# Optimization experiments

Measured on AMD Instinct MI355X. Metric: run time of the kernel, lower is better.

The kernel has to match this reference:

```python
import jax, jax.numpy as jnp
import numpy as np

B, T, D = 8, 2048, 512
F = 512          # filters (== D due to residual add)
K = 7            # kernel_size
H = 128          # hidden_dim of kernel generator (hard-coded in source)
LN_EPS = 1e-3    # keras LayerNormalization default epsilon


def setup_inputs() -> dict:
    key = jax.random.key(0)
    ks = jax.random.split(key, 8)
    x = jax.random.normal(ks[0], (B, T, D), dtype=jnp.float32)
    # kernel generator: Dense(D->H, relu) then Dense(H->K*F)
    W1 = jax.random.normal(ks[1], (D, H), dtype=jnp.float32) * (1.0 / np.sqrt(D))
    b1 = jnp.zeros((H,), dtype=jnp.float32)
    W2 = jax.random.normal(ks[2], (H, K * F), dtype=jnp.float32) * (1.0 / np.sqrt(H))
    b2 = jnp.zeros((K * F,), dtype=jnp.float32)
    # LayerNorm params
    gamma = jnp.ones((F,), dtype=jnp.float32)
    beta = jnp.zeros((F,), dtype=jnp.float32)
    return {"x": x, "W1": W1, "b1": b1, "W2": W2, "b2": b2,
            "gamma": gamma, "beta": beta}


def _dynamic_conv_block(x, W1, b1, W2, b2, gamma, beta):
    # per-token dynamic kernels: [B, T, K, F]
    h = jax.nn.relu(jnp.einsum("btd,dh->bth", x, W1) + b1)
    kernels = (jnp.einsum("bth,hf->btf", h, W2) + b2).reshape(B, T, K, F)
    # extract sliding-window patches (same padding): [B, T, K, D]
    pad = K // 2
    xp = jnp.pad(x, ((0, 0), (pad, pad), (0, 0)))
    patches = jnp.stack([xp[:, i:i + T, :] for i in range(K)], axis=2)
    # per-token conv: contract over window K and input channels D
    conv_out = jnp.einsum("btkd,btkf->btf", patches, kernels)
    # residual + LayerNorm + relu (dropout is identity at inference)
    y = conv_out + x
    mu = jnp.mean(y, axis=-1, keepdims=True)
    var = jnp.mean(jnp.square(y - mu), axis=-1, keepdims=True)
    y = (y - mu) * jax.lax.rsqrt(var + LN_EPS) * gamma + beta
    return jax.nn.relu(y)


def reference(x, W1, b1, W2, b2, gamma, beta):
    return _dynamic_conv_block(x, W1, b1, W2, b2, gamma, beta)
```

## Files before the change

### kernel.cpp

```cpp
#include <hip/hip_runtime.h>
#include <utility>

#define NT 2048
#define ND 512
#define NH 128
#define NKW 7
#define NTOK 16384

typedef float f32x4 __attribute__((ext_vector_type(4)));
typedef __bf16 bf16x8 __attribute__((ext_vector_type(8)));
typedef unsigned short u16;
typedef unsigned int u32;
typedef u16 u16x8 __attribute__((ext_vector_type(8)));

template<int N> using IC = std::integral_constant<int, N>;

__device__ __forceinline__ u16 f2bf(float f){
  u32 u = __builtin_bit_cast(u32, f);
  return (u16)((u + 0x7fffu + ((u>>16)&1u)) >> 16);
}
__device__ __forceinline__ float bf2f(u16 s){
  u32 u = ((u32)s)<<16;
  return __builtin_bit_cast(float, u);
}
__device__ __forceinline__ bf16x8 pack8(const float4& a, const float4& b){
  u16x8 u;
  u[0]=f2bf(a.x); u[1]=f2bf(a.y); u[2]=f2bf(a.z); u[3]=f2bf(a.w);
  u[4]=f2bf(b.x); u[5]=f2bf(b.y); u[6]=f2bf(b.z); u[7]=f2bf(b.w);
  return __builtin_bit_cast(bf16x8, u);
}

__global__ __launch_bounds__(256) void prep2_kernel(
    const float* __restrict__ W1, const float* __restrict__ W2,
    const float* __restrict__ b2, u16* __restrict__ W1F, u16* __restrict__ B3)
{
  int f = blockIdx.x*256 + threadIdx.x;
  u16 u[8];
  if (f < 8192){
    int n = f & 127, sk = f >> 7, kb = sk*8;
    #pragma unroll
    for (int j=0;j<8;++j) u[j] = f2bf(W1[(size_t)(kb+j)*NH + n]);
    u16x8 v;
    #pragma unroll
    for (int j=0;j<8;++j) v[j]=u[j];
    *(u16x8*)(W1F + (size_t)f*8) = v;
  } else {
    int g = f - 8192;
    int n = g & 511, sc = g >> 9, kb = sc*8;
    if (kb < 896){
      int kwin = kb >> 7, h = kb & 127;
      #pragma unroll
      for (int j=0;j<8;++j) u[j] = f2bf(W2[(size_t)(h+j)*(NKW*ND) + kwin*ND + n]);
    } else {
      int jb = kb - 896;
      #pragma unroll
      for (int j=0;j<8;++j){ int jj = jb+j; u[j] = (jj<NKW)? f2bf(b2[(size_t)jj*ND + n]) : (u16)0; }
    }
    u16x8 v;
    #pragma unroll
    for (int j=0;j<8;++j) v[j]=u[j];
    *(u16x8*)(B3 + (size_t)g*8) = v;
  }
}

__global__ __launch_bounds__(512,2) void fused_kernel(
    const float* __restrict__ x, const u16* __restrict__ W1F,
    const float* __restrict__ b1, const u16* __restrict__ B3,
    const float* __restrict__ gamma, const float* __restrict__ beta,
    float* __restrict__ out)
{
  __shared__ __align__(16) u16 h_lds[2*64*64];
  __shared__ float rs_lds[70];
  __shared__ __align__(16) float s_lds[64][8];
  __shared__ float red_s[64][8], red_q[64][8];
  __shared__ float mu_lds[64], rstd_lds[64];

  const int tid = threadIdx.x, w = tid>>6, l = tid&63;
  const int m_base = blockIdx.x*64;

  #pragma unroll
  for (int r=0;r<8;++r){
    int row = w*8 + r;
    const float4* pr = (const float4*)(x + (size_t)(m_base+row)*ND + l*8);
    float4 a = pr[0], b = pr[1];
    float s = (a.x+a.y)+(a.z+a.w)+((b.x+b.y)+(b.z+b.w));
    s += __shfl_xor(s,1); s += __shfl_xor(s,2); s += __shfl_xor(s,4);
    s += __shfl_xor(s,8); s += __shfl_xor(s,16); s += __shfl_xor(s,32);
    if (l==0) rs_lds[3+row] = s;
  }
  if (w < 6){
    int j = (w<3)? w : w+64;
    int tg2 = m_base + j - 3;
    float s2 = 0.f;
    if (tg2 >= 0 && tg2 < NTOK){
      const float4* p2 = (const float4*)(x + (size_t)tg2*ND + l*8);
      float4 a = p2[0], b = p2[1];
      s2 = (a.x+a.y)+(a.z+a.w)+((b.x+b.y)+(b.z+b.w));
    }
    s2 += __shfl_xor(s2,1); s2 += __shfl_xor(s2,2); s2 += __shfl_xor(s2,4);
    s2 += __shfl_xor(s2,8); s2 += __shfl_xor(s2,16); s2 += __shfl_xor(s2,32);
    if (l==0) rs_lds[j] = s2;
  }
  __syncthreads();
  {
    int rr = tid>>3, k = tid&7;
    float v = 0.f;
    if (k < NKW){
      int ti = (m_base+rr) & (NT-1);
      int idx = ti + k - 3;
      if (idx >= 0 && idx < NT) v = rs_lds[rr+k];
    }
    s_lds[rr][k] = v;
  }

  {
    const int wm = w>>2, wn = w&3;
    f32x4 acc1[2][2] = {};
    #pragma unroll
    for (int kc=0;kc<16;++kc){
      bf16x8 af[2], bfr[2];
      #pragma unroll
      for (int mi=0;mi<2;++mi){
        int row = wm*32 + mi*16 + (l&15);
        const float4* px = (const float4*)(x + (size_t)(m_base+row)*ND + kc*32 + (l>>4)*8);
        af[mi] = pack8(px[0], px[1]);
      }
      #pragma unroll
      for (int ni=0;ni<2;++ni){
        int n = wn*32 + ni*16 + (l&15);
        bfr[ni] = *(const bf16x8*)(W1F + ((size_t)(kc*4 + (l>>4))*128 + n)*8);
      }
      #pragma unroll
      for (int mi=0;mi<2;++mi)
        #pragma unroll
        for (int ni=0;ni<2;++ni)
          acc1[mi][ni] = __builtin_amdgcn_mfma_f32_16x16x32_bf16(af[mi], bfr[ni], acc1[mi][ni],0,0,0);
    }
    #pragma unroll
    for (int ni=0;ni<2;++ni){
      int col = wn*32 + ni*16 + (l&15);
      float bias = b1[col];
      int half = col>>6, cc = col&63;
      #pragma unroll
      for (int mi=0;mi<2;++mi)
        #pragma unroll
        for (int r=0;r<4;++r){
          int row = wm*32 + mi*16 + (l>>4)*4 + r;
          float v = fmaxf(acc1[mi][ni][r] + bias, 0.f);
          int byte = half*8192 + row*128 + ((cc*2) ^ ((row&7)<<4));
          *(u16*)((char*)h_lds + byte) = f2bf(v);
        }
    }
  }
  __syncthreads();

  f32x4 acc[4][4] = {};
  bf16x8 bE[2][4], bO[2][4];

  float sr[4][8];
  #pragma unroll
  for (int mi=0;mi<4;++mi){
    int r = mi*16 + (l&15);
    f32x4 a0 = *(const f32x4*)&s_lds[r][0];
    f32x4 a1 = *(const f32x4*)&s_lds[r][4];
    #pragma unroll
    for (int j=0;j<4;++j){ sr[mi][j] = a0[j]; sr[mi][4+j] = a1[j]; }
  }

  auto loadB = [&](int c, bf16x8 (&bf)[2][4]){
    #pragma unroll
    for (int kk=0;kk<2;++kk)
      #pragma unroll
      for (int ni=0;ni<4;++ni){
        int rowB = w*64 + ni*16 + (l&15);
        bf[kk][ni] = *(const bf16x8*)(B3 + ((size_t)((c*2+kk)*4 + (l>>4))*512 + rowB)*8);
      }
  };
  auto chunk = [&](auto kcC, bf16x8 (&b)[2][4]){
    constexpr int kc = decltype(kcC)::value;
    #pragma unroll
    for (int kk=0;kk<2;++kk){
      bf16x8 af[4];
      #pragma unroll
      for (int mi=0;mi<4;++mi){
        int r = mi*16 + (l&15);
        const char* hp = (const char*)h_lds + (kc&1)*8192 + r*128
                         + (((kk*64) + ((l>>4)*16)) ^ ((r&7)<<4));
        u16x8 hv = *(const u16x8*)hp;
        float sv = sr[mi][kc>>1];
        #pragma unroll
        for (int j=0;j<8;++j) af[mi][j] = (__bf16)(bf2f(hv[j]) * sv);
      }
      __builtin_amdgcn_s_setprio(1);
      #pragma unroll
      for (int mi=0;mi<4;++mi)
        #pragma unroll
        for (int ni=0;ni<4;++ni)
          acc[mi][ni] = __builtin_amdgcn_mfma_f32_16x16x32_bf16(af[mi], b[kk][ni], acc[mi][ni],0,0,0);
      __builtin_amdgcn_s_setprio(0);
    }
  };
  #define SB0 __builtin_amdgcn_sched_barrier(0)

  loadB(0, bE);
  SB0;
  #define PAIR(T) \
    loadB(2*(T)+1, bO); SB0; chunk(IC<2*(T)>{}, bE); \
    loadB(2*(T)+2, bE); SB0; chunk(IC<2*(T)+1>{}, bO);
  PAIR(0) PAIR(1) PAIR(2) PAIR(3) PAIR(4) PAIR(5) PAIR(6)
  #undef PAIR
  {
    bf16x8 af[4];
    const bool g0 = ((l>>4)==0);
    #pragma unroll
    for (int mi=0;mi<4;++mi){
      #pragma unroll
      for (int j=0;j<7;++j) af[mi][j] = g0 ? (__bf16)sr[mi][j] : (__bf16)0.f;
      af[mi][7] = (__bf16)0.f;
    }
    #pragma unroll
    for (int mi=0;mi<4;++mi)
      #pragma unroll
      for (int ni=0;ni<4;++ni)
        acc[mi][ni] = __builtin_amdgcn_mfma_f32_16x16x32_bf16(af[mi], bE[0][ni], acc[mi][ni],0,0,0);
  }
  #undef SB0

  #pragma unroll
  for (int mi=0;mi<4;++mi){
    #pragma unroll
    for (int r=0;r<4;++r){
      int m = mi*16 + (l>>4)*4 + r;
      int tg = m_base + m;
      float ps=0.f, pq=0.f;
      #pragma unroll
      for (int ni=0;ni<4;++ni){
        int n = w*64 + ni*16 + (l&15);
        float v = acc[mi][ni][r] + x[(size_t)tg*ND + n];
        acc[mi][ni][r] = v;
        ps += v; pq += v*v;
      }
      #pragma unroll
      for (int msk=1; msk<16; msk<<=1){ ps += __shfl_xor(ps,msk); pq += __shfl_xor(pq,msk); }
      if ((l&15)==0){ red_s[m][w]=ps; red_q[m][w]=pq; }
    }
  }
  __syncthreads();
  if (tid < 64){
    float ssum=0.f, sq=0.f;
    #pragma unroll
    for (int ww=0; ww<8; ++ww){ ssum += red_s[tid][ww]; sq += red_q[tid][ww]; }
    float mu = ssum * (1.0f/ND);
    float var = sq*(1.0f/ND) - mu*mu;
    mu_lds[tid] = mu;
    rstd_lds[tid] = rsqrtf(var + 1e-3f);
  }
  __syncthreads();
  float gv[4], bv[4];
  #pragma unroll
  for (int ni=0;ni<4;++ni){
    int n = w*64 + ni*16 + (l&15);
    gv[ni] = gamma[n]; bv[ni] = beta[n];
  }
  #pragma unroll
  for (int mi=0;mi<4;++mi){
    #pragma unroll
    for (int r=0;r<4;++r){
      int m = mi*16 + (l>>4)*4 + r;
      int tg = m_base + m;
      float mu = mu_lds[m], rstd = rstd_lds[m];
      #pragma unroll
      for (int ni=0;ni<4;++ni){
        int n = w*64 + ni*16 + (l&15);
        float v = (acc[mi][ni][r]-mu)*rstd*gv[ni] + bv[ni];
        out[(size_t)tg*ND + n] = fmaxf(v, 0.f);
      }
    }
  }
}

extern "C" void kernel_launch(void* const* d_in, const int* in_sizes, int n_in,
                              void* d_out, int out_size, void* d_ws, size_t ws_size,
                              hipStream_t stream)
{
  (void)in_sizes; (void)n_in; (void)out_size; (void)ws_size;
  const float* x     = (const float*)d_in[0];
  const float* W1    = (const float*)d_in[1];
  const float* b1    = (const float*)d_in[2];
  const float* W2    = (const float*)d_in[3];
  const float* b2    = (const float*)d_in[4];
  const float* gamma = (const float*)d_in[5];
  const float* beta  = (const float*)d_in[6];
  float* out = (float*)d_out;

  char* ws = (char*)d_ws;
  u16* W1F = (u16*)(ws);
  u16* B3  = (u16*)(ws + 131072);

  prep2_kernel<<<272, 256, 0, stream>>>(W1, W2, b2, W1F, B3);
  fused_kernel<<<256, 512, 0, stream>>>(x, W1F, b1, B3, gamma, beta, out);
}
```

Measured before the change: 140.2 us.

## Stage B3 chunks through LDS with direct global-to-LDS loads, 32-token blocks

Restructures the fused kernel to process 32 tokens per block with 256 threads across 512 blocks. The dynamic-weight matrix B3 is now staged through double-buffered LDS tiles using global_load_lds, and the scaled A operand goes through LDS, instead of each wave loading B fragments straight from global memory into registers. The goal is better latency hiding through an explicit LDS pipeline and more blocks to spread over the CUs. In exchange it uses about 70KB of LDS per block, which can limit occupancy, adds a block barrier per chunk, and halves the M-tile, so each staged B element is reused across fewer tokens.

```diff
diff --git a/kernel.cpp b/kernel.cpp
--- a/kernel.cpp
+++ b/kernel.cpp
@@ -1,5 +1,4 @@
 #include <hip/hip_runtime.h>
-#include <utility>
 
 #define NT 2048
 #define ND 512
@@ -11,9 +10,8 @@
 typedef __bf16 bf16x8 __attribute__((ext_vector_type(8)));
 typedef unsigned short u16;
 typedef unsigned int u32;
+typedef u16 u16x4 __attribute__((ext_vector_type(4)));
 typedef u16 u16x8 __attribute__((ext_vector_type(8)));
-
-template<int N> using IC = std::integral_constant<int, N>;
 
 __device__ __forceinline__ u16 f2bf(float f){
   u32 u = __builtin_bit_cast(u32, f);
@@ -28,6 +26,11 @@
   u[0]=f2bf(a.x); u[1]=f2bf(a.y); u[2]=f2bf(a.z); u[3]=f2bf(a.w);
   u[4]=f2bf(b.x); u[5]=f2bf(b.y); u[6]=f2bf(b.z); u[7]=f2bf(b.w);
   return __builtin_bit_cast(bf16x8, u);
+}
+__device__ __forceinline__ void gload_lds16(const void* g, void* l){
+  __builtin_amdgcn_global_load_lds(
+      (const __attribute__((address_space(1))) void*)g,
+      (__attribute__((address_space(3))) void*)l, 16, 0, 0);
 }
 
 __global__ __launch_bounds__(256) void prep2_kernel(
@@ -63,43 +66,34 @@
   }
 }
 
-__global__ __launch_bounds__(512,2) void fused_kernel(
+__global__ __launch_bounds__(256,2) void fused2_kernel(
     const float* __restrict__ x, const u16* __restrict__ W1F,
     const float* __restrict__ b1, const u16* __restrict__ B3,
     const float* __restrict__ gamma, const float* __restrict__ beta,
     float* __restrict__ out)
 {
-  __shared__ __align__(16) u16 h_lds[2*64*64];
-  __shared__ float rs_lds[70];
-  __shared__ __align__(16) float s_lds[64][8];
-  __shared__ float red_s[64][8], red_q[64][8];
-  __shared__ float mu_lds[64], rstd_lds[64];
+  __shared__ __align__(16) u16 Bt0[16384], Bt1[16384];
+  __shared__ __align__(16) u16 At0[1024], At1[1024];
+  __shared__ __align__(16) u16 h_lds[32*128];
+  __shared__ float rs_lds[40];
+  __shared__ float s_lds[32][8];
+  __shared__ float red_s[32][4], red_q[32][4];
+  __shared__ float mu_lds[32], rstd_lds[32];
 
   const int tid = threadIdx.x, w = tid>>6, l = tid&63;
-  const int m_base = blockIdx.x*64;
-
-  #pragma unroll
-  for (int r=0;r<8;++r){
-    int row = w*8 + r;
-    const float4* pr = (const float4*)(x + (size_t)(m_base+row)*ND + l*8);
-    float4 a = pr[0], b = pr[1];
-    float s = (a.x+a.y)+(a.z+a.w)+((b.x+b.y)+(b.z+b.w));
+  const int m_base = blockIdx.x*32;
+
+  for (int t=w; t<38; t+=4){
+    int g = m_base + t - 3;
+    float s = 0.f;
+    if (g >= 0 && g < NTOK){
+      const float4* p = (const float4*)(x + (size_t)g*ND + l*8);
+      float4 a = p[0], b = p[1];
+      s = (a.x+a.y)+(a.z+a.w)+((b.x+b.y)+(b.z+b.w));
+    }
     s += __shfl_xor(s,1); s += __shfl_xor(s,2); s += __shfl_xor(s,4);
     s += __shfl_xor(s,8); s += __shfl_xor(s,16); s += __shfl_xor(s,32);
-    if (l==0) rs_lds[3+row] = s;
-  }
-  if (w < 6){
-    int j = (w<3)? w : w+64;
-    int tg2 = m_base + j - 3;
-    float s2 = 0.f;
-    if (tg2 >= 0 && tg2 < NTOK){
-      const float4* p2 = (const float4*)(x + (size_t)tg2*ND + l*8);
-      float4 a = p2[0], b = p2[1];
-      s2 = (a.x+a.y)+(a.z+a.w)+((b.x+b.y)+(b.z+b.w));
-    }
-    s2 += __shfl_xor(s2,1); s2 += __shfl_xor(s2,2); s2 += __shfl_xor(s2,4);
-    s2 += __shfl_xor(s2,8); s2 += __shfl_xor(s2,16); s2 += __shfl_xor(s2,32);
-    if (l==0) rs_lds[j] = s2;
+    if (l==0) rs_lds[t] = s;
   }
   __syncthreads();
   {
@@ -114,164 +108,155 @@
   }
 
   {
-    const int wm = w>>2, wn = w&3;
-    f32x4 acc1[2][2] = {};
+    const int wm = w&1, wn = w>>1;
+    f32x4 acc1[4] = {};
     #pragma unroll
     for (int kc=0;kc<16;++kc){
-      bf16x8 af[2], bfr[2];
-      #pragma unroll
-      for (int mi=0;mi<2;++mi){
-        int row = wm*32 + mi*16 + (l&15);
-        const float4* px = (const float4*)(x + (size_t)(m_base+row)*ND + kc*32 + (l>>4)*8);
-        af[mi] = pack8(px[0], px[1]);
-      }
-      #pragma unroll
-      for (int ni=0;ni<2;++ni){
-        int n = wn*32 + ni*16 + (l&15);
-        bfr[ni] = *(const bf16x8*)(W1F + ((size_t)(kc*4 + (l>>4))*128 + n)*8);
-      }
-      #pragma unroll
-      for (int mi=0;mi<2;++mi)
-        #pragma unroll
-        for (int ni=0;ni<2;++ni)
-          acc1[mi][ni] = __builtin_amdgcn_mfma_f32_16x16x32_bf16(af[mi], bfr[ni], acc1[mi][ni],0,0,0);
-    }
-    #pragma unroll
-    for (int ni=0;ni<2;++ni){
-      int col = wn*32 + ni*16 + (l&15);
+      int row = wm*16 + (l&15);
+      const float4* px = (const float4*)(x + (size_t)(m_base+row)*ND + kc*32 + (l>>4)*8);
+      bf16x8 af = pack8(px[0], px[1]);
+      #pragma unroll
+      for (int ni=0;ni<4;++ni){
+        int n = wn*64 + ni*16 + (l&15);
+        bf16x8 bfr = *(const bf16x8*)(W1F + ((size_t)(kc*4+(l>>4))*128 + n)*8);
+        acc1[ni] = __builtin_amdgcn_mfma_f32_16x16x32_bf16(af, bfr, acc1[ni],0,0,0);
+      }
+    }
+    #pragma unroll
+    for (int ni=0;ni<4;++ni){
+      int col = wn*64 + ni*16 + (l&15);
       float bias = b1[col];
-      int half = col>>6, cc = col&63;
-      #pragma unroll
-      for (int mi=0;mi<2;++mi)
-        #pragma unroll
-        for (int r=0;r<4;++r){
-          int row = wm*32 + mi*16 + (l>>4)*4 + r;
-          float v = fmaxf(acc1[mi][ni][r] + bias, 0.f);
-          int byte = half*8192 + row*128 + ((cc*2) ^ ((row&7)<<4));
-          *(u16*)((char*)h_lds + byte) = f2bf(v);
-        }
-    }
-  }
-  __syncthreads();
-
-  f32x4 acc[4][4] = {};
-  bf16x8 bE[2][4], bO[2][4];
-
-  float sr[4][8];
-  #pragma unroll
-  for (int mi=0;mi<4;++mi){
-    int r = mi*16 + (l&15);
-    f32x4 a0 = *(const f32x4*)&s_lds[r][0];
-    f32x4 a1 = *(const f32x4*)&s_lds[r][4];
-    #pragma unroll
-    for (int j=0;j<4;++j){ sr[mi][j] = a0[j]; sr[mi][4+j] = a1[j]; }
-  }
-
-  auto loadB = [&](int c, bf16x8 (&bf)[2][4]){
-    #pragma unroll
-    for (int kk=0;kk<2;++kk)
-      #pragma unroll
-      for (int ni=0;ni<4;++ni){
-        int rowB = w*64 + ni*16 + (l&15);
-        bf[kk][ni] = *(const bf16x8*)(B3 + ((size_t)((c*2+kk)*4 + (l>>4))*512 + rowB)*8);
-      }
-  };
-  auto chunk = [&](auto kcC, bf16x8 (&b)[2][4]){
-    constexpr int kc = decltype(kcC)::value;
-    #pragma unroll
-    for (int kk=0;kk<2;++kk){
-      bf16x8 af[4];
-      #pragma unroll
-      for (int mi=0;mi<4;++mi){
-        int r = mi*16 + (l&15);
-        const char* hp = (const char*)h_lds + (kc&1)*8192 + r*128
-                         + (((kk*64) + ((l>>4)*16)) ^ ((r&7)<<4));
-        u16x8 hv = *(const u16x8*)hp;
-        float sv = sr[mi][kc>>1];
-        #pragma unroll
-        for (int j=0;j<8;++j) af[mi][j] = (__bf16)(bf2f(hv[j]) * sv);
-      }
-      __builtin_amdgcn_s_setprio(1);
-      #pragma unroll
-      for (int mi=0;mi<4;++mi)
-        #pragma unroll
-        for (int ni=0;ni<4;++ni)
-          acc[mi][ni] = __builtin_amdgcn_mfma_f32_16x16x32_bf16(af[mi], b[kk][ni], acc[mi][ni],0,0,0);
-      __builtin_amdgcn_s_setprio(0);
-    }
-  };
-  #define SB0 __builtin_amdgcn_sched_barrier(0)
-
-  loadB(0, bE);
-  SB0;
-  #define PAIR(T) \
-    loadB(2*(T)+1, bO); SB0; chunk(IC<2*(T)>{}, bE); \
-    loadB(2*(T)+2, bE); SB0; chunk(IC<2*(T)+1>{}, bO);
-  PAIR(0) PAIR(1) PAIR(2) PAIR(3) PAIR(4) PAIR(5) PAIR(6)
-  #undef PAIR
-  {
-    bf16x8 af[4];
-    const bool g0 = ((l>>4)==0);
-    #pragma unroll
-    for (int mi=0;mi<4;++mi){
-      #pragma unroll
-      for (int j=0;j<7;++j) af[mi][j] = g0 ? (__bf16)sr[mi][j] : (__bf16)0.f;
-      af[mi][7] = (__bf16)0.f;
-    }
-    #pragma unroll
-    for (int mi=0;mi<4;++mi)
-      #pragma unroll
-      for (int ni=0;ni<4;++ni)
-        acc[mi][ni] = __builtin_amdgcn_mfma_f32_16x16x32_bf16(af[mi], bE[0][ni], acc[mi][ni],0,0,0);
-  }
-  #undef SB0
-
-  #pragma unroll
-  for (int mi=0;mi<4;++mi){
+      #pragma unroll
+      for (int r=0;r<4;++r){
+        int row = wm*16 + (l>>4)*4 + r;
+        float v = fmaxf(acc1[ni][r] + bias, 0.f);
+        int byte = row*256 + ((2*col) ^ ((row&7)<<4));
+        *(u16*)((char*)h_lds + byte) = f2bf(v);
+      }
+    }
+  }
+  __syncthreads();
+
+  f32x4 acc[2][8] = {};
+  const int srow = (tid>>1)&31, shalf = tid&1;
+  const int s_rowbase = srow*256, s_xor = (srow&7)<<4;
+
+  auto stageB = [&](int c, u16* dstB){
+    #pragma unroll
+    for (int i=0;i<8;++i){
+      int seg = w*8 + i;
+      const char* g = (const char*)B3 + (size_t)c*32768 + seg*1024 + l*16;
+      gload_lds16(g, (char*)dstB + seg*1024);
+    }
+  };
+  auto stageA = [&](int c, u16* dstA){
+    float sv = s_lds[srow][c>>2];
+    int slotbyte = (c&3)*64 + w*16;
+    u16x4 hv = *(const u16x4*)((const char*)h_lds + s_rowbase + (slotbyte ^ s_xor) + shalf*8);
+    u16x4 o;
+    #pragma unroll
+    for (int j=0;j<4;++j) o[j] = f2bf(bf2f(hv[j]) * sv);
+    *(u16x4*)(dstA + tid*4) = o;
+  };
+  auto stageAbias = [&](u16* dstA){
+    u16x4 o;
+    #pragma unroll
+    for (int j=0;j<4;++j){
+      float v = 0.f;
+      if (w==0){
+        int k = shalf*4 + j;
+        if (k < NKW) v = s_lds[srow][k];
+      }
+      o[j] = f2bf(v);
+    }
+    *(u16x4*)(dstA + tid*4) = o;
+  };
+  auto mfmaC = [&](const u16* A, const u16* B){
+    int abase = ((l>>4)*32 + (l&15))*8;
+    bf16x8 af0 = *(const bf16x8*)(A + abase);
+    bf16x8 af1 = *(const bf16x8*)(A + abase + 16*8);
+    int bbase = ((l>>4)*512 + w*128 + (l&15))*8;
+    __builtin_amdgcn_s_setprio(1);
+    #pragma unroll
+    for (int ni=0;ni<8;++ni){
+      bf16x8 bf = *(const bf16x8*)(B + bbase + ni*16*8);
+      acc[0][ni] = __builtin_amdgcn_mfma_f32_16x16x32_bf16(af0, bf, acc[0][ni],0,0,0);
+      acc[1][ni] = __builtin_amdgcn_mfma_f32_16x16x32_bf16(af1, bf, acc[1][ni],0,0,0);
+    }
+    __builtin_amdgcn_s_setprio(0);
+  };
+
+  stageB(0, Bt0);
+  stageA(0, At0);
+  __syncthreads();
+  #pragma unroll
+  for (int t=0;t<14;++t){
+    stageB(2*t+1, Bt1);
+    __builtin_amdgcn_sched_barrier(0);
+    stageA(2*t+1, At1);
+    mfmaC(At0, Bt0);
+    __syncthreads();
+    if (t < 13){
+      stageB(2*t+2, Bt0);
+      __builtin_amdgcn_sched_barrier(0);
+      stageA(2*t+2, At0);
+    } else {
+      stageB(28, Bt0);
+      __builtin_amdgcn_sched_barrier(0);
+      stageAbias(At0);
+    }
+    mfmaC(At1, Bt1);
+    __syncthreads();
+  }
+  mfmaC(At0, Bt0);
+
+  float gv[8], bv[8];
+  #pragma unroll
+  for (int ni=0;ni<8;++ni){
+    int n = w*128 + ni*16 + (l&15);
+    gv[ni] = gamma[n]; bv[ni] = beta[n];
+  }
+  #pragma unroll
+  for (int mi=0;mi<2;++mi){
     #pragma unroll
     for (int r=0;r<4;++r){
       int m = mi*16 + (l>>4)*4 + r;
       int tg = m_base + m;
       float ps=0.f, pq=0.f;
       #pragma unroll
-      for (int ni=0;ni<4;++ni){
-        int n = w*64 + ni*16 + (l&15);
+      for (int ni=0;ni<8;++ni){
+        int n = w*128 + ni*16 + (l&15);
         float v = acc[mi][ni][r] + x[(size_t)tg*ND + n];
         acc[mi][ni][r] = v;
         ps += v; pq += v*v;
       }
-      #pragma unroll
-      for (int msk=1; msk<16; msk<<=1){ ps += __shfl_xor(ps,msk); pq += __shfl_xor(pq,msk); }
+      ps += __shfl_xor(ps,1); pq += __shfl_xor(pq,1);
+      ps += __shfl_xor(ps,2); pq += __shfl_xor(pq,2);
+      ps += __shfl_xor(ps,4); pq += __shfl_xor(pq,4);
+      ps += __shfl_xor(ps,8); pq += __shfl_xor(pq,8);
       if ((l&15)==0){ red_s[m][w]=ps; red_q[m][w]=pq; }
     }
   }
   __syncthreads();
-  if (tid < 64){
-    float ssum=0.f, sq=0.f;
-    #pragma unroll
-    for (int ww=0; ww<8; ++ww){ ssum += red_s[tid][ww]; sq += red_q[tid][ww]; }
+  if (tid < 32){
+    float ssum = red_s[tid][0]+red_s[tid][1]+red_s[tid][2]+red_s[tid][3];
+    float sq   = red_q[tid][0]+red_q[tid][1]+red_q[tid][2]+red_q[tid][3];
     float mu = ssum * (1.0f/ND);
     float var = sq*(1.0f/ND) - mu*mu;
     mu_lds[tid] = mu;
     rstd_lds[tid] = rsqrtf(var + 1e-3f);
   }
   __syncthreads();
-  float gv[4], bv[4];
-  #pragma unroll
-  for (int ni=0;ni<4;++ni){
-    int n = w*64 + ni*16 + (l&15);
-    gv[ni] = gamma[n]; bv[ni] = beta[n];
-  }
-  #pragma unroll
-  for (int mi=0;mi<4;++mi){
+  #pragma unroll
+  for (int mi=0;mi<2;++mi){
     #pragma unroll
     for (int r=0;r<4;++r){
       int m = mi*16 + (l>>4)*4 + r;
       int tg = m_base + m;
       float mu = mu_lds[m], rstd = rstd_lds[m];
       #pragma unroll
-      for (int ni=0;ni<4;++ni){
-        int n = w*64 + ni*16 + (l&15);
+      for (int ni=0;ni<8;++ni){
+        int n = w*128 + ni*16 + (l&15);
         float v = (acc[mi][ni][r]-mu)*rstd*gv[ni] + bv[ni];
         out[(size_t)tg*ND + n] = fmaxf(v, 0.f);
       }
@@ -298,5 +283,5 @@
   u16* B3  = (u16*)(ws + 131072);
 
   prep2_kernel<<<272, 256, 0, stream>>>(W1, W2, b2, W1F, B3);
-  fused_kernel<<<256, 512, 0, stream>>>(x, W1F, b1, B3, gamma, beta, out);
-}
+  fused2_kernel<<<512, 256, 0, stream>>>(x, W1F, b1, B3, gamma, beta, out);
+}
```

Result: no change. 140.2 us (+0.0%).
